# Performance work log

Hardware: AMD Instinct MI355X
Metric: run time of the kernel (lower is better)

The kernel has to match this reference:

```python
import jax, jax.numpy as jnp
from jax import lax
import numpy as np

B, T, NX, NXS, NY, NYS, H = 4096, 60, 4, 3, 4, 3, 128


def lstm(x, h0, c0, Wih, Whh, bih, bhh):
    """PyTorch-convention LSTM. x: [B,T,D] -> (hs [B,T,H], hT, cT). Gate order i,f,g,o."""
    xg = jnp.einsum('btd,gd->btg', x, Wih) + bih  # [B,T,4H] precomputed input gates

    def step(carry, xg_t):
        h, c = carry
        g = xg_t + h @ Whh.T + bhh
        i, f, gg, o = jnp.split(g, 4, axis=-1)
        c = jax.nn.sigmoid(f) * c + jax.nn.sigmoid(i) * jnp.tanh(gg)
        h = jax.nn.sigmoid(o) * jnp.tanh(c)
        return (h, c), h

    (hT, cT), hs = lax.scan(step, (h0, c0), jnp.swapaxes(xg, 0, 1))
    return jnp.swapaxes(hs, 0, 1), hT, cT


def setup_inputs() -> dict:
    key = jax.random.key(0)
    ks = jax.random.split(key, 24)
    s = 0.1  # weight init scale
    inp = {
        'inputs_main': jax.random.normal(ks[0], (B, T, NX), jnp.float32),
        'inputs_sfc': jax.random.normal(ks[1], (B, NXS), jnp.float32),
        'rnn1_mem': jax.random.normal(ks[2], (B, T, H), jnp.float32),
        'hx2': jax.random.normal(ks[3], (B, H), jnp.float32),
        'cx2': jax.random.normal(ks[4], (B, H), jnp.float32),
        # surface MLPs -> initial h/c of rnn1
        'W_sfc1': s * jax.random.normal(ks[5], (H, NXS), jnp.float32),
        'b_sfc1': s * jax.random.normal(ks[6], (H,), jnp.float32),
        'W_sfc2': s * jax.random.normal(ks[7], (H, NXS), jnp.float32),
        'b_sfc2': s * jax.random.normal(ks[8], (H,), jnp.float32),
        # rnn1: input dim nx + nh_mem = 4 + 128 = 132
        'Wih1': s * jax.random.normal(ks[9], (4 * H, NX + H), jnp.float32),
        'Whh1': s * jax.random.normal(ks[10], (4 * H, H), jnp.float32),
        'bih1': s * jax.random.normal(ks[11], (4 * H,), jnp.float32),
        'bhh1': s * jax.random.normal(ks[12], (4 * H,), jnp.float32),
        # rnn2: input dim H
        'Wih2': s * jax.random.normal(ks[13], (4 * H, H), jnp.float32),
        'Whh2': s * jax.random.normal(ks[14], (4 * H, H), jnp.float32),
        'bih2': s * jax.random.normal(ks[15], (4 * H,), jnp.float32),
        'bhh2': s * jax.random.normal(ks[16], (4 * H,), jnp.float32),
        # intermediate + output MLPs
        'W_lat': s * jax.random.normal(ks[17], (H, H), jnp.float32),
        'b_lat': s * jax.random.normal(ks[18], (H,), jnp.float32),
        'W_out': s * jax.random.normal(ks[19], (NY, H), jnp.float32),
        'b_out': s * jax.random.normal(ks[20], (NY,), jnp.float32),
        'W_so': s * jax.random.normal(ks[21], (NYS, H), jnp.float32),
        'b_so': s * jax.random.normal(ks[22], (NYS,), jnp.float32),
    }
    return inp


def reference(inputs_main, inputs_sfc, rnn1_mem, hx2, cx2,
              W_sfc1, b_sfc1, W_sfc2, b_sfc2,
              Wih1, Whh1, bih1, bhh1,
              Wih2, Whh2, bih2, bhh2,
              W_lat, b_lat, W_out, b_out, W_so, b_so):
    # initial states of rnn1 from surface features
    hx = jnp.tanh(inputs_sfc @ W_sfc1.T + b_sfc1)
    cx = jnp.tanh(inputs_sfc @ W_sfc2.T + b_sfc2)
    # flip vertical levels, concat memory feedback
    x = jnp.flip(inputs_main, axis=1)
    x = jnp.concatenate([x, rnn1_mem], axis=2)  # [B,T,NX+H]
    rnn1out, _, _ = lstm(x, hx, cx, Wih1, Whh1, bih1, bhh1)
    rnn1out = jnp.flip(rnn1out, axis=1)
    # second LSTM over the opposite direction, random initial state
    rnn2out, last_h, _ = lstm(rnn1out, hx2, cx2, Wih2, Whh2, bih2, bhh2)
    # intermediate mlp (also becomes next-step memory in the stateful module)
    lat = rnn2out @ W_lat.T + b_lat  # [B,T,H]
    out = lat @ W_out.T + b_out      # [B,T,NY]
    out_sfc = last_h @ W_so.T + b_so  # [B,NYS]
    return out, out_sfc
```

## Files before the change

kernel.cpp:

```cpp
#include <hip/hip_runtime.h>
#include <stdint.h>


typedef __bf16 bf16x8 __attribute__((ext_vector_type(8)));
typedef __bf16 bf16x4 __attribute__((ext_vector_type(4)));
typedef float  f32x4  __attribute__((ext_vector_type(4)));

#define HQ      4096u
#define H0_OFF  0u
#define XD_OFF  8192u
#define XA_OFF  24576u
#define HIST    32256u
#define LDS_SZ  163328
#define NWS     28

#define S1f (-1.4426950408889634f)
#define S2f (-2.8853900817779268f)

__device__ __forceinline__ bf16x8 ldw8s(const float* __restrict__ p, float s){
  float4 a = *(const float4*)p;
  float4 b = *(const float4*)(p+4);
  bf16x8 r;
  r[0]=(__bf16)(a.x*s); r[1]=(__bf16)(a.y*s); r[2]=(__bf16)(a.z*s); r[3]=(__bf16)(a.w*s);
  r[4]=(__bf16)(b.x*s); r[5]=(__bf16)(b.y*s); r[6]=(__bf16)(b.z*s); r[7]=(__bf16)(b.w*s);
  return r;
}
__device__ __forceinline__ void load_wgate(bf16x8 (&dst)[8], const float* pih, const float* phh, int gg, float s){
  #pragma unroll
  for (int kk=0;kk<4;++kk) dst[kk]   = ldw8s(pih + kk*32 + gg*8, s);
  #pragma unroll
  for (int kk=0;kk<4;++kk) dst[4+kk] = ldw8s(phh + kk*32 + gg*8, s);
}
__device__ __forceinline__ void step_barrier(){
  asm volatile("s_waitcnt lgkmcnt(0)\n\ts_barrier" ::: "memory");
}
__device__ __forceinline__ void lstm_pw(const f32x4& a0, const f32x4& a1,
                                        const f32x4& a2, const f32x4& a3,
                                        float (&c_)[4], float (&hn)[4]){
  #pragma unroll
  for (int i=0;i<4;++i){
    float ei = __builtin_amdgcn_exp2f(a0[i]);
    float ef = __builtin_amdgcn_exp2f(a1[i]);
    float eg = __builtin_amdgcn_exp2f(fminf(a2[i], 126.0f));
    float eo = __builtin_amdgcn_exp2f(a3[i]);
    float sf = __builtin_amdgcn_rcpf(1.0f + ef);
    float itg = (1.0f - eg) * __builtin_amdgcn_rcpf((1.0f + ei)*(1.0f + eg));
    float ci = sf*c_[i] + itg;
    float ec = __builtin_amdgcn_exp2f(S2f*__builtin_fabsf(ci));
    float th = (1.0f - ec) * __builtin_amdgcn_rcpf((1.0f + eo)*(1.0f + ec));
    c_[i] = ci;
    hn[i] = __builtin_copysignf(th, ci);
  }
}

__global__ void comb_kernel(const float* __restrict__ W_lat, const float* __restrict__ b_lat,
                            const float* __restrict__ W_out, const float* __restrict__ b_out,
                            float* __restrict__ wcomb){
  int tid = threadIdx.x;
  int m = tid >> 7, k = tid & 127;
  float s = 0.f;
  for (int a=0;a<128;++a) s += W_out[m*128+a]*W_lat[a*128+k];
  wcomb[tid] = s;
  if (tid < 4){
    float sb = b_out[tid];
    for (int a=0;a<128;++a) sb += W_out[tid*128+a]*b_lat[a];
    wcomb[512+tid] = sb;
  }
}

#define MF(af_,wb_,ac_) ac_ = __builtin_amdgcn_mfma_f32_16x16x32_bf16(af_, wb_, ac_, 0,0,0)

#define XPART1(A0_,A1_,A2_,A3_, XB_, TT_) do{ \
    bf16x8 xa_ = {}; \
    if (gg == 0){ bf16x4 x4_ = *(const bf16x4*)(lds + XA_OFF + (uint32_t)((((TT_))<<4)+l16)*8u); \
      xa_[0]=x4_[0]; xa_[1]=x4_[1]; xa_[2]=x4_[2]; xa_[3]=x4_[3]; } \
    A0_ = (f32x4){bias0,bias0,bias0,bias0}; \
    A1_ = (f32x4){bias1,bias1,bias1,bias1}; \
    A2_ = (f32x4){bias2,bias2,bias2,bias2}; \
    A3_ = (f32x4){bias3,bias3,bias3,bias3}; \
    MF(xa_,wxB0,A0_); MF(xa_,wxB1,A1_); MF(xa_,wxB2,A2_); MF(xa_,wxB3,A3_); \
    _Pragma("unroll") \
    for (int kk_=0;kk_<4;++kk_){ \
      uint4 q_ = *(const uint4*)(lds + (XB_) + ((abase + 64u*(uint32_t)kk_) ^ amask)); \
      bf16x8 af_ = __builtin_bit_cast(bf16x8, q_); \
      MF(af_,wB0[kk_],A0_); MF(af_,wB1[kk_],A1_); MF(af_,wB2[kk_],A2_); MF(af_,wB3[kk_],A3_); } \
  }while(0)

#define XPART2(A0_,A1_,A2_,A3_, XB_) do{ \
    A0_ = (f32x4){bias0,bias0,bias0,bias0}; \
    A1_ = (f32x4){bias1,bias1,bias1,bias1}; \
    A2_ = (f32x4){bias2,bias2,bias2,bias2}; \
    A3_ = (f32x4){bias3,bias3,bias3,bias3}; \
    _Pragma("unroll") \
    for (int kk_=0;kk_<4;++kk_){ \
      uint4 q_ = *(const uint4*)(lds + (XB_) + ((abase + 64u*(uint32_t)kk_) ^ amask)); \
      bf16x8 af_ = __builtin_bit_cast(bf16x8, q_); \
      MF(af_,wB0[kk_],A0_); MF(af_,wB1[kk_],A1_); MF(af_,wB2[kk_],A2_); MF(af_,wB3[kk_],A3_); } \
  }while(0)

#define BODY1(T_, CUR_, C0,C1,C2,C3, N0,N1,N2,N3) { \
    const uint32_t Hc_ = H0_OFF + (uint32_t)(CUR_)*HQ; \
    uint4 qh0_ = *(const uint4*)(lds + Hc_ + ((abase       ) ^ amask)); \
    uint4 qh1_ = *(const uint4*)(lds + Hc_ + ((abase +  64u) ^ amask)); \
    uint4 qh2_ = *(const uint4*)(lds + Hc_ + ((abase + 128u) ^ amask)); \
    uint4 qh3_ = *(const uint4*)(lds + Hc_ + ((abase + 192u) ^ amask)); \
    uint2 hv_ = *(const uint2*)(lds + Hc_ + stg_off); \
    if ((T_) < 59){ \
      const int s1_ = (T_) + 1; \
      const uint32_t xb_ = (s1_ >= NWS) ? (HIST + (uint32_t)(s1_-NWS)*HQ) : (XD_OFF + (uint32_t)(s1_&3)*HQ); \
      XPART1(N0,N1,N2,N3, xb_, 58-(T_)); \
    } \
    bf16x8 h0_ = __builtin_bit_cast(bf16x8, qh0_); \
    bf16x8 h1_ = __builtin_bit_cast(bf16x8, qh1_); \
    bf16x8 h2_ = __builtin_bit_cast(bf16x8, qh2_); \
    bf16x8 h3_ = __builtin_bit_cast(bf16x8, qh3_); \
    MF(h0_,wB0[4],C0); MF(h0_,wB1[4],C1); MF(h0_,wB2[4],C2); MF(h0_,wB3[4],C3); \
    MF(h1_,wB0[5],C0); MF(h1_,wB1[5],C1); MF(h1_,wB2[5],C2); MF(h1_,wB3[5],C3); \
    MF(h2_,wB0[6],C0); MF(h2_,wB1[6],C1); MF(h2_,wB2[6],C2); MF(h2_,wB3[6],C3); \
    MF(h3_,wB0[7],C0); MF(h3_,wB1[7],C1); MF(h3_,wB2[7],C2); MF(h3_,wB3[7],C3); \
    float hn_[4]; \
    lstm_pw(C0,C1,C2,C3, c_, hn_); \
    if ((T_) >= 1){ \
      if ((T_) <= NWS) ws_u2[ws_base + (size_t)((T_)-1)*512 + tid] = hv_; \
      else *(uint2*)(lds + HIST + (uint32_t)((T_)-1-NWS)*HQ + stg_off) = hv_; \
    } \
    if ((T_) + 2 <= 59){ \
      const int s2_ = (T_) + 2; \
      const uint32_t sd_ = (s2_ >= NWS) ? (HIST + (uint32_t)(s2_-NWS)*HQ) : (XD_OFF + (uint32_t)(s2_&3)*HQ); \
      bf16x4 m4_; m4_[0]=(__bf16)P0.x; m4_[1]=(__bf16)P0.y; m4_[2]=(__bf16)P0.z; m4_[3]=(__bf16)P0.w; \
      *(bf16x4*)(lds + sd_ + stg_off) = m4_; \
    } \
    _Pragma("unroll") \
    for (int i_=0;i_<4;++i_) \
      *(__bf16*)(lds + H0_OFF + (uint32_t)(1-(CUR_))*HQ + hw_off[i_]) = (__bf16)hn_[i_]; \
    P0 = P1; \
    if ((T_) + 4 <= 59) P1 = *(const float4*)(memrow + (size_t)((T_)+4)*128); \
    step_barrier(); \
  }

#define BODY2(T_, CUR_, C0,C1,C2,C3, N0,N1,N2,N3) { \
    const uint32_t Hc_ = H0_OFF + (uint32_t)(CUR_)*HQ; \
    uint4 qh0_ = *(const uint4*)(lds + Hc_ + ((abase       ) ^ amask)); \
    uint4 qh1_ = *(const uint4*)(lds + Hc_ + ((abase +  64u) ^ amask)); \
    uint4 qh2_ = *(const uint4*)(lds + Hc_ + ((abase + 128u) ^ amask)); \
    uint4 qh3_ = *(const uint4*)(lds + Hc_ + ((abase + 192u) ^ amask)); \
    if ((T_) < 59){ \
      const int s1_ = 58 - (T_); \
      const uint32_t xb_ = (s1_ >= NWS) ? (HIST + (uint32_t)(s1_-NWS)*HQ) : (XD_OFF + (uint32_t)(s1_&3)*HQ); \
      XPART2(N0,N1,N2,N3, xb_); \
    } \
    bf16x8 h0_ = __builtin_bit_cast(bf16x8, qh0_); \
    bf16x8 h1_ = __builtin_bit_cast(bf16x8, qh1_); \
    bf16x8 h2_ = __builtin_bit_cast(bf16x8, qh2_); \
    bf16x8 h3_ = __builtin_bit_cast(bf16x8, qh3_); \
    MF(h0_,wB0[4],C0); MF(h0_,wB1[4],C1); MF(h0_,wB2[4],C2); MF(h0_,wB3[4],C3); \
    MF(h1_,wB0[5],C0); MF(h1_,wB1[5],C1); MF(h1_,wB2[5],C2); MF(h1_,wB3[5],C3); \
    MF(h2_,wB0[6],C0); MF(h2_,wB1[6],C1); MF(h2_,wB2[6],C2); MF(h2_,wB3[6],C3); \
    MF(h3_,wB0[7],C0); MF(h3_,wB1[7],C1); MF(h3_,wB2[7],C2); MF(h3_,wB3[7],C3); \
    f32x4 ao_ = {0.f,0.f,0.f,0.f}; \
    if (w == 0){ MF(h0_,wcB[0],ao_); MF(h1_,wcB[1],ao_); MF(h2_,wcB[2],ao_); MF(h3_,wcB[3],ao_); } \
    float hn_[4]; \
    lstm_pw(C0,C1,C2,C3, c_, hn_); \
    if ((T_) > 0 && w == 0 && l16 < 4){ \
      _Pragma("unroll") \
      for (int i_=0;i_<4;++i_) \
        dout[(size_t)(b0 + gg*4 + i_)*240 + (size_t)((T_)-1)*4 + l16] = ao_[i_] + bc; \
    } \
    if ((T_) >= 29 && (T_) <= 56) \
      *(uint2*)(lds + XD_OFF + (uint32_t)((56-(T_))&3)*HQ + stg_off) = P0u; \
    _Pragma("unroll") \
    for (int i_=0;i_<4;++i_) \
      *(__bf16*)(lds + H0_OFF + (uint32_t)(1-(CUR_))*HQ + hw_off[i_]) = (__bf16)hn_[i_]; \
    P0u = P1u; \
    if ((T_) >= 27 && (T_) <= 54) P1u = ws_u2[ws_base + (size_t)(54-(T_))*512 + tid]; \
    step_barrier(); \
  }

__global__ __launch_bounds__(512, 2)
void lstm_fused(const float* __restrict__ xmain_g, const float* __restrict__ sfc,
                const float* __restrict__ mem_g, const float* __restrict__ hx2g,
                const float* __restrict__ cx2g,
                const float* __restrict__ Wsfc1, const float* __restrict__ bsfc1,
                const float* __restrict__ Wsfc2, const float* __restrict__ bsfc2,
                const float* __restrict__ Wih1, const float* __restrict__ Whh1,
                const float* __restrict__ bih1, const float* __restrict__ bhh1,
                const float* __restrict__ Wih2, const float* __restrict__ Whh2,
                const float* __restrict__ bih2, const float* __restrict__ bhh2,
                const float* __restrict__ Wso, const float* __restrict__ bso,
                const float* __restrict__ wcomb_ws,
                uint2* __restrict__ ws_u2, float* __restrict__ dout)
{
  __shared__ __align__(16) unsigned char lds[LDS_SZ];
  const int tid = threadIdx.x;
  const int w   = tid >> 6;
  const int l   = tid & 63;
  const int gg  = l >> 4;
  const int l16 = l & 15;
  const int blk = blockIdx.x;
  const int b0  = blk * 16;
  const int j   = (w<<4) + l16;
  const uint32_t amask = (uint32_t)((l16 & 7) << 4);
  const uint32_t abase = (uint32_t)(l16*256 + gg*16);
  const int srow = tid >> 5;
  const uint32_t stg_off = (uint32_t)(((srow*256) + (tid&31)*8) ^ ((srow&7)<<4));
  uint32_t hw_off[4];
  #pragma unroll
  for (int i=0;i<4;++i){
    int r = gg*4 + i;
    hw_off[i] = (uint32_t)((r*256 + j*2) ^ ((r&7)<<4));
  }
  const size_t ws_base = (size_t)blk * NWS * 512;

  #pragma unroll
  for (int e = tid; e < 960; e += 512){
    int t = e >> 4, row = e & 15;
    float4 xv = *(const float4*)(xmain_g + (size_t)(b0+row)*240 + t*4);
    bf16x4 b4; b4[0]=(__bf16)xv.x; b4[1]=(__bf16)xv.y; b4[2]=(__bf16)xv.z; b4[3]=(__bf16)xv.w;
    *(bf16x4*)(lds + XA_OFF + (uint32_t)e*8u) = b4;
  }
  const float* memrow = mem_g + (size_t)(b0 + srow)*7680 + (tid&31)*4;
  {
    float4 m0 = *(const float4*)memrow;
    float4 m1 = *(const float4*)(memrow + 128);
    bf16x4 a4; a4[0]=(__bf16)m0.x; a4[1]=(__bf16)m0.y; a4[2]=(__bf16)m0.z; a4[3]=(__bf16)m0.w;
    bf16x4 b4; b4[0]=(__bf16)m1.x; b4[1]=(__bf16)m1.y; b4[2]=(__bf16)m1.z; b4[3]=(__bf16)m1.w;
    *(bf16x4*)(lds + XD_OFF + stg_off) = a4;
    *(bf16x4*)(lds + XD_OFF + HQ + stg_off) = b4;
  }
  {
    int c0 = (tid&31)*4;
    float4 wa = *(const float4*)(Wsfc1 + c0*3);
    float4 wb = *(const float4*)(Wsfc1 + c0*3 + 4);
    float4 wc = *(const float4*)(Wsfc1 + c0*3 + 8);
    const float* sp = sfc + (size_t)(b0+srow)*3;
    float s0 = sp[0], s1 = sp[1], s2 = sp[2];
    float4 bb = *(const float4*)(bsfc1 + c0);
    float v0 = tanhf(bb.x + s0*wa.x + s1*wa.y + s2*wa.z);
    float v1 = tanhf(bb.y + s0*wa.w + s1*wb.x + s2*wb.y);
    float v2 = tanhf(bb.z + s0*wb.z + s1*wb.w + s2*wc.x);
    float v3 = tanhf(bb.w + s0*wc.y + s1*wc.z + s2*wc.w);
    bf16x4 h4; h4[0]=(__bf16)v0; h4[1]=(__bf16)v1; h4[2]=(__bf16)v2; h4[3]=(__bf16)v3;
    *(bf16x4*)(lds + H0_OFF + stg_off) = h4;
  }
  float c_[4];
  {
    const float* wr = Wsfc2 + j*3;
    float w0_=wr[0], w1_=wr[1], w2_=wr[2];
    float bj = bsfc2[j];
    #pragma unroll
    for (int i=0;i<4;++i){
      const float* sp = sfc + (size_t)(b0 + gg*4 + i)*3;
      c_[i] = tanhf(bj + sp[0]*w0_ + sp[1]*w1_ + sp[2]*w2_);
    }
  }
  bf16x8 wB0[8], wB1[8], wB2[8], wB3[8];
  load_wgate(wB0, Wih1 + 4 + (size_t)(0*128+j)*132, Whh1 + (size_t)(0*128+j)*128, gg, S1f);
  load_wgate(wB1, Wih1 + 4 + (size_t)(1*128+j)*132, Whh1 + (size_t)(1*128+j)*128, gg, S1f);
  load_wgate(wB2, Wih1 + 4 + (size_t)(2*128+j)*132, Whh1 + (size_t)(2*128+j)*128, gg, S2f);
  load_wgate(wB3, Wih1 + 4 + (size_t)(3*128+j)*132, Whh1 + (size_t)(3*128+j)*128, gg, S1f);
  bf16x8 wxB0 = {}, wxB1 = {}, wxB2 = {}, wxB3 = {};
  if (gg == 0){
    float4 x0 = *(const float4*)(Wih1 + (size_t)(0*128+j)*132);
    float4 x1 = *(const float4*)(Wih1 + (size_t)(1*128+j)*132);
    float4 x2 = *(const float4*)(Wih1 + (size_t)(2*128+j)*132);
    float4 x3 = *(const float4*)(Wih1 + (size_t)(3*128+j)*132);
    wxB0[0]=(__bf16)(x0.x*S1f); wxB0[1]=(__bf16)(x0.y*S1f); wxB0[2]=(__bf16)(x0.z*S1f); wxB0[3]=(__bf16)(x0.w*S1f);
    wxB1[0]=(__bf16)(x1.x*S1f); wxB1[1]=(__bf16)(x1.y*S1f); wxB1[2]=(__bf16)(x1.z*S1f); wxB1[3]=(__bf16)(x1.w*S1f);
    wxB2[0]=(__bf16)(x2.x*S2f); wxB2[1]=(__bf16)(x2.y*S2f); wxB2[2]=(__bf16)(x2.z*S2f); wxB2[3]=(__bf16)(x2.w*S2f);
    wxB3[0]=(__bf16)(x3.x*S1f); wxB3[1]=(__bf16)(x3.y*S1f); wxB3[2]=(__bf16)(x3.z*S1f); wxB3[3]=(__bf16)(x3.w*S1f);
  }
  float bias0 = (bih1[0*128+j] + bhh1[0*128+j])*S1f;
  float bias1 = (bih1[1*128+j] + bhh1[1*128+j])*S1f;
  float bias2 = (bih1[2*128+j] + bhh1[2*128+j])*S2f;
  float bias3 = (bih1[3*128+j] + bhh1[3*128+j])*S1f;
  float4 P0 = *(const float4*)(memrow + 2*128);
  float4 P1 = *(const float4*)(memrow + 3*128);
  step_barrier();

  f32x4 A0, A1, A2, A3, B0, B1, B2, B3;
  XPART1(A0,A1,A2,A3, XD_OFF, 59);

  #pragma unroll 1
  for (int tb = 0; tb < 60; tb += 2){
    BODY1(tb,   0, A0,A1,A2,A3, B0,B1,B2,B3)
    BODY1(tb+1, 1, B0,B1,B2,B3, A0,A1,A2,A3)
  }
  {
    uint2 hv = *(const uint2*)(lds + H0_OFF + stg_off);
    *(uint2*)(lds + HIST + 31u*HQ + stg_off) = hv;
    float4 h2v = *(const float4*)(hx2g + (size_t)(b0+srow)*128 + (tid&31)*4);
    bf16x4 h4; h4[0]=(__bf16)h2v.x; h4[1]=(__bf16)h2v.y; h4[2]=(__bf16)h2v.z; h4[3]=(__bf16)h2v.w;
    *(bf16x4*)(lds + H0_OFF + stg_off) = h4;
  }
  #pragma unroll
  for (int i=0;i<4;++i) c_[i] = cx2g[(size_t)(b0 + gg*4 + i)*128 + j];
  load_wgate(wB0, Wih2 + (size_t)(0*128+j)*128, Whh2 + (size_t)(0*128+j)*128, gg, S1f);
  load_wgate(wB1, Wih2 + (size_t)(1*128+j)*128, Whh2 + (size_t)(1*128+j)*128, gg, S1f);
  load_wgate(wB2, Wih2 + (size_t)(2*128+j)*128, Whh2 + (size_t)(2*128+j)*128, gg, S2f);
  load_wgate(wB3, Wih2 + (size_t)(3*128+j)*128, Whh2 + (size_t)(3*128+j)*128, gg, S1f);
  float nb0 = (bih2[0*128+j] + bhh2[0*128+j])*S1f;
  float nb1 = (bih2[1*128+j] + bhh2[1*128+j])*S1f;
  float nb2 = (bih2[2*128+j] + bhh2[2*128+j])*S2f;
  float nb3 = (bih2[3*128+j] + bhh2[3*128+j])*S1f;
  bias0=nb0; bias1=nb1; bias2=nb2; bias3=nb3;
  bf16x8 wcB[4] = {};
  if (w == 0){
    #pragma unroll
    for (int kk=0;kk<4;++kk){
      bf16x8 v = {};
      if (l16 < 4) v = ldw8s(wcomb_ws + l16*128 + kk*32 + gg*8, 1.0f);
      wcB[kk] = v;
    }
  }
  const float bc = (l16 < 4) ? wcomb_ws[512 + l16] : 0.f;
  asm volatile("s_waitcnt vmcnt(0) lgkmcnt(0)" ::: "memory");
  __builtin_amdgcn_s_barrier();

  uint2 P0u, P1u;
  XPART2(A0,A1,A2,A3, HIST + 31u*HQ);

  #pragma unroll 1
  for (int tb = 0; tb < 60; tb += 2){
    BODY2(tb,   0, A0,A1,A2,A3, B0,B1,B2,B3)
    BODY2(tb+1, 1, B0,B1,B2,B3, A0,A1,A2,A3)
  }

  if (w == 0){
    bf16x8 wsB[4];
    #pragma unroll
    for (int kk=0;kk<4;++kk){
      bf16x8 v = {};
      if (l16 < 3) v = ldw8s(Wso + l16*128 + kk*32 + gg*8, 1.0f);
      wsB[kk] = v;
    }
    f32x4 ao = {0.f,0.f,0.f,0.f};
    f32x4 as_ = {0.f,0.f,0.f,0.f};
    #pragma unroll
    for (int kk=0;kk<4;++kk){
      uint4 q = *(const uint4*)(lds + H0_OFF + ((abase + 64u*(uint32_t)kk) ^ amask));
      bf16x8 af = __builtin_bit_cast(bf16x8, q);
      ao  = __builtin_amdgcn_mfma_f32_16x16x32_bf16(af, wcB[kk], ao, 0,0,0);
      as_ = __builtin_amdgcn_mfma_f32_16x16x32_bf16(af, wsB[kk], as_, 0,0,0);
    }
    if (l16 < 4){
      #pragma unroll
      for (int i=0;i<4;++i)
        dout[(size_t)(b0 + gg*4 + i)*240 + 59*4 + l16] = ao[i] + bc;
    }
    if (l16 < 3){
      float bs = bso[l16];
      #pragma unroll
      for (int i=0;i<4;++i)
        dout[983040 + (size_t)(b0 + gg*4 + i)*3 + l16] = as_[i] + bs;
    }
  }
}

extern "C" void kernel_launch(void* const* d_in, const int* in_sizes, int n_in,
                              void* d_out, int out_size, void* d_ws, size_t ws_size,
                              hipStream_t stream){
  const float* inputs_main = (const float*)d_in[0];
  const float* inputs_sfc  = (const float*)d_in[1];
  const float* rnn1_mem    = (const float*)d_in[2];
  const float* hx2  = (const float*)d_in[3];
  const float* cx2  = (const float*)d_in[4];
  const float* W_sfc1 = (const float*)d_in[5];
  const float* b_sfc1 = (const float*)d_in[6];
  const float* W_sfc2 = (const float*)d_in[7];
  const float* b_sfc2 = (const float*)d_in[8];
  const float* Wih1 = (const float*)d_in[9];
  const float* Whh1 = (const float*)d_in[10];
  const float* bih1 = (const float*)d_in[11];
  const float* bhh1 = (const float*)d_in[12];
  const float* Wih2 = (const float*)d_in[13];
  const float* Whh2 = (const float*)d_in[14];
  const float* bih2 = (const float*)d_in[15];
  const float* bhh2 = (const float*)d_in[16];
  const float* W_lat = (const float*)d_in[17];
  const float* b_lat = (const float*)d_in[18];
  const float* W_out = (const float*)d_in[19];
  const float* b_out = (const float*)d_in[20];
  const float* W_so  = (const float*)d_in[21];
  const float* b_so  = (const float*)d_in[22];
  float* out = (float*)d_out;
  uint2* ws_u2 = (uint2*)d_ws;
  float* wcomb = (float*)((char*)d_ws + 62914560u);

  comb_kernel<<<dim3(1), dim3(512), 0, stream>>>(W_lat, b_lat, W_out, b_out, wcomb);
  lstm_fused<<<dim3(256), dim3(512), 0, stream>>>(inputs_main, inputs_sfc, rnn1_mem, hx2, cx2,
      W_sfc1, b_sfc1, W_sfc2, b_sfc2, Wih1, Whh1, bih1, bhh1, Wih2, Whh2, bih2, bhh2,
      W_so, b_so, wcomb, ws_u2, out);
}
```

Measured before the change: 198.5 us.

## Spill layer-1 hidden history to global workspace and drop LDS history buffer

Layer 1's hidden-state history now goes entirely to a per-block global workspace, row-major, instead of being split between workspace and a large LDS history region. This shrinks LDS from about 160KB to about 32KB. Layer 2 reads its inputs straight from workspace into registers, two steps ahead. The input-projection MFMAs are no longer precomputed one step early; they run in the same step as the recurrent MFMAs. That puts more MFMA work and LDS reads on each step's critical path, in exchange for smaller LDS and simpler indexing.

```diff
diff --git a/kernel.cpp b/kernel.cpp
--- a/kernel.cpp
+++ b/kernel.cpp
@@ -10,9 +10,7 @@
 #define H0_OFF  0u
 #define XD_OFF  8192u
 #define XA_OFF  24576u
-#define HIST    32256u
-#define LDS_SZ  163328
-#define NWS     28
+#define LDS_SZ  32256
 
 #define S1f (-1.4426950408889634f)
 #define S2f (-2.8853900817779268f)
@@ -69,110 +67,41 @@
 }
 
 #define MF(af_,wb_,ac_) ac_ = __builtin_amdgcn_mfma_f32_16x16x32_bf16(af_, wb_, ac_, 0,0,0)
-
-#define XPART1(A0_,A1_,A2_,A3_, XB_, TT_) do{ \
-    bf16x8 xa_ = {}; \
-    if (gg == 0){ bf16x4 x4_ = *(const bf16x4*)(lds + XA_OFF + (uint32_t)((((TT_))<<4)+l16)*8u); \
-      xa_[0]=x4_[0]; xa_[1]=x4_[1]; xa_[2]=x4_[2]; xa_[3]=x4_[3]; } \
-    A0_ = (f32x4){bias0,bias0,bias0,bias0}; \
-    A1_ = (f32x4){bias1,bias1,bias1,bias1}; \
-    A2_ = (f32x4){bias2,bias2,bias2,bias2}; \
-    A3_ = (f32x4){bias3,bias3,bias3,bias3}; \
-    MF(xa_,wxB0,A0_); MF(xa_,wxB1,A1_); MF(xa_,wxB2,A2_); MF(xa_,wxB3,A3_); \
-    _Pragma("unroll") \
-    for (int kk_=0;kk_<4;++kk_){ \
-      uint4 q_ = *(const uint4*)(lds + (XB_) + ((abase + 64u*(uint32_t)kk_) ^ amask)); \
-      bf16x8 af_ = __builtin_bit_cast(bf16x8, q_); \
-      MF(af_,wB0[kk_],A0_); MF(af_,wB1[kk_],A1_); MF(af_,wB2[kk_],A2_); MF(af_,wB3[kk_],A3_); } \
-  }while(0)
-
-#define XPART2(A0_,A1_,A2_,A3_, XB_) do{ \
-    A0_ = (f32x4){bias0,bias0,bias0,bias0}; \
-    A1_ = (f32x4){bias1,bias1,bias1,bias1}; \
-    A2_ = (f32x4){bias2,bias2,bias2,bias2}; \
-    A3_ = (f32x4){bias3,bias3,bias3,bias3}; \
-    _Pragma("unroll") \
-    for (int kk_=0;kk_<4;++kk_){ \
-      uint4 q_ = *(const uint4*)(lds + (XB_) + ((abase + 64u*(uint32_t)kk_) ^ amask)); \
-      bf16x8 af_ = __builtin_bit_cast(bf16x8, q_); \
-      MF(af_,wB0[kk_],A0_); MF(af_,wB1[kk_],A1_); MF(af_,wB2[kk_],A2_); MF(af_,wB3[kk_],A3_); } \
-  }while(0)
-
-#define BODY1(T_, CUR_, C0,C1,C2,C3, N0,N1,N2,N3) { \
+#define BC8(q_) __builtin_bit_cast(bf16x8, q_)
+
+#define BODY2(T_, CUR_, X0_,X1_,X2_,X3_) { \
     const uint32_t Hc_ = H0_OFF + (uint32_t)(CUR_)*HQ; \
     uint4 qh0_ = *(const uint4*)(lds + Hc_ + ((abase       ) ^ amask)); \
     uint4 qh1_ = *(const uint4*)(lds + Hc_ + ((abase +  64u) ^ amask)); \
     uint4 qh2_ = *(const uint4*)(lds + Hc_ + ((abase + 128u) ^ amask)); \
     uint4 qh3_ = *(const uint4*)(lds + Hc_ + ((abase + 192u) ^ amask)); \
-    uint2 hv_ = *(const uint2*)(lds + Hc_ + stg_off); \
-    if ((T_) < 59){ \
-      const int s1_ = (T_) + 1; \
-      const uint32_t xb_ = (s1_ >= NWS) ? (HIST + (uint32_t)(s1_-NWS)*HQ) : (XD_OFF + (uint32_t)(s1_&3)*HQ); \
-      XPART1(N0,N1,N2,N3, xb_, 58-(T_)); \
+    f32x4 a0 = biasv0, a1 = biasv1, a2 = biasv2, a3 = biasv3; \
+    MF(BC8(X0_),wB0[0],a0); MF(BC8(X0_),wB1[0],a1); MF(BC8(X0_),wB2[0],a2); MF(BC8(X0_),wB3[0],a3); \
+    MF(BC8(X1_),wB0[1],a0); MF(BC8(X1_),wB1[1],a1); MF(BC8(X1_),wB2[1],a2); MF(BC8(X1_),wB3[1],a3); \
+    MF(BC8(X2_),wB0[2],a0); MF(BC8(X2_),wB1[2],a1); MF(BC8(X2_),wB2[2],a2); MF(BC8(X2_),wB3[2],a3); \
+    MF(BC8(X3_),wB0[3],a0); MF(BC8(X3_),wB1[3],a1); MF(BC8(X3_),wB2[3],a2); MF(BC8(X3_),wB3[3],a3); \
+    if ((T_) <= 57){ \
+      const char* xp_ = wsb + (size_t)(57-(T_))*4096u + xfoff; \
+      X0_ = *(const uint4*)(xp_);      X1_ = *(const uint4*)(xp_+64); \
+      X2_ = *(const uint4*)(xp_+128);  X3_ = *(const uint4*)(xp_+192); \
     } \
-    bf16x8 h0_ = __builtin_bit_cast(bf16x8, qh0_); \
-    bf16x8 h1_ = __builtin_bit_cast(bf16x8, qh1_); \
-    bf16x8 h2_ = __builtin_bit_cast(bf16x8, qh2_); \
-    bf16x8 h3_ = __builtin_bit_cast(bf16x8, qh3_); \
-    MF(h0_,wB0[4],C0); MF(h0_,wB1[4],C1); MF(h0_,wB2[4],C2); MF(h0_,wB3[4],C3); \
-    MF(h1_,wB0[5],C0); MF(h1_,wB1[5],C1); MF(h1_,wB2[5],C2); MF(h1_,wB3[5],C3); \
-    MF(h2_,wB0[6],C0); MF(h2_,wB1[6],C1); MF(h2_,wB2[6],C2); MF(h2_,wB3[6],C3); \
-    MF(h3_,wB0[7],C0); MF(h3_,wB1[7],C1); MF(h3_,wB2[7],C2); MF(h3_,wB3[7],C3); \
-    float hn_[4]; \
-    lstm_pw(C0,C1,C2,C3, c_, hn_); \
-    if ((T_) >= 1){ \
-      if ((T_) <= NWS) ws_u2[ws_base + (size_t)((T_)-1)*512 + tid] = hv_; \
-      else *(uint2*)(lds + HIST + (uint32_t)((T_)-1-NWS)*HQ + stg_off) = hv_; \
-    } \
-    if ((T_) + 2 <= 59){ \
-      const int s2_ = (T_) + 2; \
-      const uint32_t sd_ = (s2_ >= NWS) ? (HIST + (uint32_t)(s2_-NWS)*HQ) : (XD_OFF + (uint32_t)(s2_&3)*HQ); \
-      bf16x4 m4_; m4_[0]=(__bf16)P0.x; m4_[1]=(__bf16)P0.y; m4_[2]=(__bf16)P0.z; m4_[3]=(__bf16)P0.w; \
-      *(bf16x4*)(lds + sd_ + stg_off) = m4_; \
-    } \
-    _Pragma("unroll") \
-    for (int i_=0;i_<4;++i_) \
-      *(__bf16*)(lds + H0_OFF + (uint32_t)(1-(CUR_))*HQ + hw_off[i_]) = (__bf16)hn_[i_]; \
-    P0 = P1; \
-    if ((T_) + 4 <= 59) P1 = *(const float4*)(memrow + (size_t)((T_)+4)*128); \
-    step_barrier(); \
-  }
-
-#define BODY2(T_, CUR_, C0,C1,C2,C3, N0,N1,N2,N3) { \
-    const uint32_t Hc_ = H0_OFF + (uint32_t)(CUR_)*HQ; \
-    uint4 qh0_ = *(const uint4*)(lds + Hc_ + ((abase       ) ^ amask)); \
-    uint4 qh1_ = *(const uint4*)(lds + Hc_ + ((abase +  64u) ^ amask)); \
-    uint4 qh2_ = *(const uint4*)(lds + Hc_ + ((abase + 128u) ^ amask)); \
-    uint4 qh3_ = *(const uint4*)(lds + Hc_ + ((abase + 192u) ^ amask)); \
-    if ((T_) < 59){ \
-      const int s1_ = 58 - (T_); \
-      const uint32_t xb_ = (s1_ >= NWS) ? (HIST + (uint32_t)(s1_-NWS)*HQ) : (XD_OFF + (uint32_t)(s1_&3)*HQ); \
-      XPART2(N0,N1,N2,N3, xb_); \
-    } \
-    bf16x8 h0_ = __builtin_bit_cast(bf16x8, qh0_); \
-    bf16x8 h1_ = __builtin_bit_cast(bf16x8, qh1_); \
-    bf16x8 h2_ = __builtin_bit_cast(bf16x8, qh2_); \
-    bf16x8 h3_ = __builtin_bit_cast(bf16x8, qh3_); \
-    MF(h0_,wB0[4],C0); MF(h0_,wB1[4],C1); MF(h0_,wB2[4],C2); MF(h0_,wB3[4],C3); \
-    MF(h1_,wB0[5],C0); MF(h1_,wB1[5],C1); MF(h1_,wB2[5],C2); MF(h1_,wB3[5],C3); \
-    MF(h2_,wB0[6],C0); MF(h2_,wB1[6],C1); MF(h2_,wB2[6],C2); MF(h2_,wB3[6],C3); \
-    MF(h3_,wB0[7],C0); MF(h3_,wB1[7],C1); MF(h3_,wB2[7],C2); MF(h3_,wB3[7],C3); \
+    bf16x8 h0_ = BC8(qh0_), h1_ = BC8(qh1_), h2_ = BC8(qh2_), h3_ = BC8(qh3_); \
+    MF(h0_,wB0[4],a0); MF(h0_,wB1[4],a1); MF(h0_,wB2[4],a2); MF(h0_,wB3[4],a3); \
+    MF(h1_,wB0[5],a0); MF(h1_,wB1[5],a1); MF(h1_,wB2[5],a2); MF(h1_,wB3[5],a3); \
+    MF(h2_,wB0[6],a0); MF(h2_,wB1[6],a1); MF(h2_,wB2[6],a2); MF(h2_,wB3[6],a3); \
+    MF(h3_,wB0[7],a0); MF(h3_,wB1[7],a1); MF(h3_,wB2[7],a2); MF(h3_,wB3[7],a3); \
     f32x4 ao_ = {0.f,0.f,0.f,0.f}; \
     if (w == 0){ MF(h0_,wcB[0],ao_); MF(h1_,wcB[1],ao_); MF(h2_,wcB[2],ao_); MF(h3_,wcB[3],ao_); } \
     float hn_[4]; \
-    lstm_pw(C0,C1,C2,C3, c_, hn_); \
+    lstm_pw(a0,a1,a2,a3, c_, hn_); \
     if ((T_) > 0 && w == 0 && l16 < 4){ \
       _Pragma("unroll") \
       for (int i_=0;i_<4;++i_) \
         dout[(size_t)(b0 + gg*4 + i_)*240 + (size_t)((T_)-1)*4 + l16] = ao_[i_] + bc; \
     } \
-    if ((T_) >= 29 && (T_) <= 56) \
-      *(uint2*)(lds + XD_OFF + (uint32_t)((56-(T_))&3)*HQ + stg_off) = P0u; \
     _Pragma("unroll") \
     for (int i_=0;i_<4;++i_) \
       *(__bf16*)(lds + H0_OFF + (uint32_t)(1-(CUR_))*HQ + hw_off[i_]) = (__bf16)hn_[i_]; \
-    P0u = P1u; \
-    if ((T_) >= 27 && (T_) <= 54) P1u = ws_u2[ws_base + (size_t)(54-(T_))*512 + tid]; \
     step_barrier(); \
   }
 
@@ -209,7 +138,10 @@
     int r = gg*4 + i;
     hw_off[i] = (uint32_t)((r*256 + j*2) ^ ((r&7)<<4));
   }
-  const size_t ws_base = (size_t)blk * NWS * 512;
+  uint2* wsimg = ws_u2 + (size_t)blk * 30720;
+  const uint32_t imgoff = (uint32_t)(srow*32 + (tid&31));
+  const char* wsb = (const char*)(ws_u2 + (size_t)blk * 30720);
+  const uint32_t xfoff = (uint32_t)(l16*256 + gg*16);
 
   #pragma unroll
   for (int e = tid; e < 960; e += 512){
@@ -273,21 +205,61 @@
   float bias1 = (bih1[1*128+j] + bhh1[1*128+j])*S1f;
   float bias2 = (bih1[2*128+j] + bhh1[2*128+j])*S2f;
   float bias3 = (bih1[3*128+j] + bhh1[3*128+j])*S1f;
+  f32x4 biasv0 = {bias0,bias0,bias0,bias0};
+  f32x4 biasv1 = {bias1,bias1,bias1,bias1};
+  f32x4 biasv2 = {bias2,bias2,bias2,bias2};
+  f32x4 biasv3 = {bias3,bias3,bias3,bias3};
   float4 P0 = *(const float4*)(memrow + 2*128);
   float4 P1 = *(const float4*)(memrow + 3*128);
   step_barrier();
 
-  f32x4 A0, A1, A2, A3, B0, B1, B2, B3;
-  XPART1(A0,A1,A2,A3, XD_OFF, 59);
-
   #pragma unroll 1
-  for (int tb = 0; tb < 60; tb += 2){
-    BODY1(tb,   0, A0,A1,A2,A3, B0,B1,B2,B3)
-    BODY1(tb+1, 1, B0,B1,B2,B3, A0,A1,A2,A3)
+  for (int t=0; t<60; ++t){
+    const uint32_t cur = (uint32_t)(t & 1);
+    const uint32_t Hc = H0_OFF + cur*HQ;
+    const uint32_t xb = XD_OFF + (uint32_t)(t & 3)*HQ;
+    uint4 qx0 = *(const uint4*)(lds + xb + ((abase       ) ^ amask));
+    uint4 qx1 = *(const uint4*)(lds + xb + ((abase +  64u) ^ amask));
+    uint4 qx2 = *(const uint4*)(lds + xb + ((abase + 128u) ^ amask));
+    uint4 qx3 = *(const uint4*)(lds + xb + ((abase + 192u) ^ amask));
+    uint4 qh0 = *(const uint4*)(lds + Hc + ((abase       ) ^ amask));
+    uint4 qh1 = *(const uint4*)(lds + Hc + ((abase +  64u) ^ amask));
+    uint4 qh2 = *(const uint4*)(lds + Hc + ((abase + 128u) ^ amask));
+    uint4 qh3 = *(const uint4*)(lds + Hc + ((abase + 192u) ^ amask));
+    uint2 hv  = *(const uint2*)(lds + Hc + stg_off);
+    bf16x8 xa = {};
+    if (gg == 0){
+      bf16x4 x4 = *(const bf16x4*)(lds + XA_OFF + (uint32_t)(((59-t)<<4) + l16)*8u);
+      xa[0]=x4[0]; xa[1]=x4[1]; xa[2]=x4[2]; xa[3]=x4[3];
+    }
+    f32x4 a0 = biasv0, a1 = biasv1, a2 = biasv2, a3 = biasv3;
+    MF(xa,wxB0,a0); MF(xa,wxB1,a1); MF(xa,wxB2,a2); MF(xa,wxB3,a3);
+    MF(BC8(qx0),wB0[0],a0); MF(BC8(qx0),wB1[0],a1); MF(BC8(qx0),wB2[0],a2); MF(BC8(qx0),wB3[0],a3);
+    MF(BC8(qx1),wB0[1],a0); MF(BC8(qx1),wB1[1],a1); MF(BC8(qx1),wB2[1],a2); MF(BC8(qx1),wB3[1],a3);
+    MF(BC8(qx2),wB0[2],a0); MF(BC8(qx2),wB1[2],a1); MF(BC8(qx2),wB2[2],a2); MF(BC8(qx2),wB3[2],a3);
+    MF(BC8(qx3),wB0[3],a0); MF(BC8(qx3),wB1[3],a1); MF(BC8(qx3),wB2[3],a2); MF(BC8(qx3),wB3[3],a3);
+    bf16x8 h0 = BC8(qh0), h1 = BC8(qh1), h2 = BC8(qh2), h3 = BC8(qh3);
+    MF(h0,wB0[4],a0); MF(h0,wB1[4],a1); MF(h0,wB2[4],a2); MF(h0,wB3[4],a3);
+    MF(h1,wB0[5],a0); MF(h1,wB1[5],a1); MF(h1,wB2[5],a2); MF(h1,wB3[5],a3);
+    MF(h2,wB0[6],a0); MF(h2,wB1[6],a1); MF(h2,wB2[6],a2); MF(h2,wB3[6],a3);
+    MF(h3,wB0[7],a0); MF(h3,wB1[7],a1); MF(h3,wB2[7],a2); MF(h3,wB3[7],a3);
+    float hn[4];
+    lstm_pw(a0,a1,a2,a3, c_, hn);
+    if (t >= 1) wsimg[(size_t)(t-1)*512 + imgoff] = hv;
+    if (t + 2 <= 59){
+      bf16x4 m4; m4[0]=(__bf16)P0.x; m4[1]=(__bf16)P0.y; m4[2]=(__bf16)P0.z; m4[3]=(__bf16)P0.w;
+      *(bf16x4*)(lds + XD_OFF + (uint32_t)((t+2)&3)*HQ + stg_off) = m4;
+    }
+    #pragma unroll
+    for (int i=0;i<4;++i)
+      *(__bf16*)(lds + H0_OFF + (1u-cur)*HQ + hw_off[i]) = (__bf16)hn[i];
+    P0 = P1;
+    if (t + 4 <= 59) P1 = *(const float4*)(memrow + (size_t)(t+4)*128);
+    step_barrier();
   }
   {
     uint2 hv = *(const uint2*)(lds + H0_OFF + stg_off);
-    *(uint2*)(lds + HIST + 31u*HQ + stg_off) = hv;
+    wsimg[(size_t)59*512 + imgoff] = hv;
     float4 h2v = *(const float4*)(hx2g + (size_t)(b0+srow)*128 + (tid&31)*4);
     bf16x4 h4; h4[0]=(__bf16)h2v.x; h4[1]=(__bf16)h2v.y; h4[2]=(__bf16)h2v.z; h4[3]=(__bf16)h2v.w;
     *(bf16x4*)(lds + H0_OFF + stg_off) = h4;
@@ -298,11 +270,16 @@
   load_wgate(wB1, Wih2 + (size_t)(1*128+j)*128, Whh2 + (size_t)(1*128+j)*128, gg, S1f);
   load_wgate(wB2, Wih2 + (size_t)(2*128+j)*128, Whh2 + (size_t)(2*128+j)*128, gg, S2f);
   load_wgate(wB3, Wih2 + (size_t)(3*128+j)*128, Whh2 + (size_t)(3*128+j)*128, gg, S1f);
-  float nb0 = (bih2[0*128+j] + bhh2[0*128+j])*S1f;
-  float nb1 = (bih2[1*128+j] + bhh2[1*128+j])*S1f;
-  float nb2 = (bih2[2*128+j] + bhh2[2*128+j])*S2f;
-  float nb3 = (bih2[3*128+j] + bhh2[3*128+j])*S1f;
-  bias0=nb0; bias1=nb1; bias2=nb2; bias3=nb3;
+  {
+    float nb0 = (bih2[0*128+j] + bhh2[0*128+j])*S1f;
+    float nb1 = (bih2[1*128+j] + bhh2[1*128+j])*S1f;
+    float nb2 = (bih2[2*128+j] + bhh2[2*128+j])*S2f;
+    float nb3 = (bih2[3*128+j] + bhh2[3*128+j])*S1f;
+    biasv0 = (f32x4){nb0,nb0,nb0,nb0};
+    biasv1 = (f32x4){nb1,nb1,nb1,nb1};
+    biasv2 = (f32x4){nb2,nb2,nb2,nb2};
+    biasv3 = (f32x4){nb3,nb3,nb3,nb3};
+  }
   bf16x8 wcB[4] = {};
   if (w == 0){
     #pragma unroll
@@ -316,13 +293,20 @@
   asm volatile("s_waitcnt vmcnt(0) lgkmcnt(0)" ::: "memory");
   __builtin_amdgcn_s_barrier();
 
-  uint2 P0u, P1u;
-  XPART2(A0,A1,A2,A3, HIST + 31u*HQ);
+  uint4 xA0, xA1, xA2, xA3, xB0t, xB1t, xB2t, xB3t;
+  {
+    const char* pa = wsb + (size_t)59*4096u + xfoff;
+    const char* pb = wsb + (size_t)58*4096u + xfoff;
+    xA0 = *(const uint4*)(pa);     xA1 = *(const uint4*)(pa+64);
+    xA2 = *(const uint4*)(pa+128); xA3 = *(const uint4*)(pa+192);
+    xB0t = *(const uint4*)(pb);     xB1t = *(const uint4*)(pb+64);
+    xB2t = *(const uint4*)(pb+128); xB3t = *(const uint4*)(pb+192);
+  }
 
   #pragma unroll 1
   for (int tb = 0; tb < 60; tb += 2){
-    BODY2(tb,   0, A0,A1,A2,A3, B0,B1,B2,B3)
-    BODY2(tb+1, 1, B0,B1,B2,B3, A0,A1,A2,A3)
+    BODY2(tb,   0, xA0,xA1,xA2,xA3)
+    BODY2(tb+1, 1, xB0t,xB1t,xB2t,xB3t)
   }
 
   if (w == 0){
@@ -338,9 +322,9 @@
     #pragma unroll
     for (int kk=0;kk<4;++kk){
       uint4 q = *(const uint4*)(lds + H0_OFF + ((abase + 64u*(uint32_t)kk) ^ amask));
-      bf16x8 af = __builtin_bit_cast(bf16x8, q);
-      ao  = __builtin_amdgcn_mfma_f32_16x16x32_bf16(af, wcB[kk], ao, 0,0,0);
-      as_ = __builtin_amdgcn_mfma_f32_16x16x32_bf16(af, wsB[kk], as_, 0,0,0);
+      bf16x8 af = BC8(q);
+      MF(af, wcB[kk], ao);
+      MF(af, wsB[kk], as_);
     }
     if (l16 < 4){
       #pragma unroll
```

After: 228.0 us. 1.15x slower.

## Prefetch next-step input fragments from LDS into registers across the barrier

Applied to the files above, without the earlier changes.

Each LSTM step now issues the LDS reads for the input-projection operands of step t+2 right before the barrier. The barrier waits only on the older LDS ops via a partial lgkmcnt wait, so those reads overlap the barrier and the next step's recurrent MFMAs instead of sitting on the critical path. To keep this safe, the staging of the memory input is pushed one step further ahead, and the prologue stages three slots. This costs extra registers (two sets of uint4 fragments) and relies on exact lgkmcnt counts, which could cause hazards or spills under the 2-block launch bound.

```diff
diff --git a/kernel.cpp b/kernel.cpp
--- a/kernel.cpp
+++ b/kernel.cpp
@@ -31,9 +31,11 @@
   #pragma unroll
   for (int kk=0;kk<4;++kk) dst[4+kk] = ldw8s(phh + kk*32 + gg*8, s);
 }
-__device__ __forceinline__ void step_barrier(){
-  asm volatile("s_waitcnt lgkmcnt(0)\n\ts_barrier" ::: "memory");
-}
+#define BAR0() asm volatile("s_waitcnt lgkmcnt(0)\n\ts_barrier" ::: "memory")
+#define BAR4() asm volatile("s_waitcnt lgkmcnt(4)\n\ts_barrier" ::: "memory")
+#define BAR5() asm volatile("s_waitcnt lgkmcnt(5)\n\ts_barrier" ::: "memory")
+__device__ __forceinline__ void step_barrier(){ BAR0(); }
+
 __device__ __forceinline__ void lstm_pw(const f32x4& a0, const f32x4& a1,
                                         const f32x4& a2, const f32x4& a3,
                                         float (&c_)[4], float (&hn)[4]){
@@ -69,6 +71,14 @@
 }
 
 #define MF(af_,wb_,ac_) ac_ = __builtin_amdgcn_mfma_f32_16x16x32_bf16(af_, wb_, ac_, 0,0,0)
+#define BC8(q_) __builtin_bit_cast(bf16x8, q_)
+#define XSLOT(s_) (((s_) >= NWS) ? (HIST + (uint32_t)((s_)-NWS)*HQ) : (XD_OFF + (uint32_t)((s_)&3)*HQ))
+
+#define PF(X0_,X1_,X2_,X3_, SLOT_) { \
+    X0_ = *(const uint4*)(lds + (SLOT_) + ((abase       ) ^ amask)); \
+    X1_ = *(const uint4*)(lds + (SLOT_) + ((abase +  64u) ^ amask)); \
+    X2_ = *(const uint4*)(lds + (SLOT_) + ((abase + 128u) ^ amask)); \
+    X3_ = *(const uint4*)(lds + (SLOT_) + ((abase + 192u) ^ amask)); }
 
 #define XPART1(A0_,A1_,A2_,A3_, XB_, TT_) do{ \
     bf16x8 xa_ = {}; \
@@ -82,7 +92,7 @@
     _Pragma("unroll") \
     for (int kk_=0;kk_<4;++kk_){ \
       uint4 q_ = *(const uint4*)(lds + (XB_) + ((abase + 64u*(uint32_t)kk_) ^ amask)); \
-      bf16x8 af_ = __builtin_bit_cast(bf16x8, q_); \
+      bf16x8 af_ = BC8(q_); \
       MF(af_,wB0[kk_],A0_); MF(af_,wB1[kk_],A1_); MF(af_,wB2[kk_],A2_); MF(af_,wB3[kk_],A3_); } \
   }while(0)
 
@@ -94,26 +104,44 @@
     _Pragma("unroll") \
     for (int kk_=0;kk_<4;++kk_){ \
       uint4 q_ = *(const uint4*)(lds + (XB_) + ((abase + 64u*(uint32_t)kk_) ^ amask)); \
-      bf16x8 af_ = __builtin_bit_cast(bf16x8, q_); \
+      bf16x8 af_ = BC8(q_); \
       MF(af_,wB0[kk_],A0_); MF(af_,wB1[kk_],A1_); MF(af_,wB2[kk_],A2_); MF(af_,wB3[kk_],A3_); } \
   }while(0)
 
-#define BODY1(T_, CUR_, C0,C1,C2,C3, N0,N1,N2,N3) { \
+#define XPART1R(A0_,A1_,A2_,A3_, X0_,X1_,X2_,X3_, XAV_) do{ \
+    bf16x8 xa_ = {}; \
+    if (gg == 0){ xa_[0]=(XAV_)[0]; xa_[1]=(XAV_)[1]; xa_[2]=(XAV_)[2]; xa_[3]=(XAV_)[3]; } \
+    A0_ = (f32x4){bias0,bias0,bias0,bias0}; \
+    A1_ = (f32x4){bias1,bias1,bias1,bias1}; \
+    A2_ = (f32x4){bias2,bias2,bias2,bias2}; \
+    A3_ = (f32x4){bias3,bias3,bias3,bias3}; \
+    MF(xa_,wxB0,A0_); MF(xa_,wxB1,A1_); MF(xa_,wxB2,A2_); MF(xa_,wxB3,A3_); \
+    MF(BC8(X0_),wB0[0],A0_); MF(BC8(X0_),wB1[0],A1_); MF(BC8(X0_),wB2[0],A2_); MF(BC8(X0_),wB3[0],A3_); \
+    MF(BC8(X1_),wB0[1],A0_); MF(BC8(X1_),wB1[1],A1_); MF(BC8(X1_),wB2[1],A2_); MF(BC8(X1_),wB3[1],A3_); \
+    MF(BC8(X2_),wB0[2],A0_); MF(BC8(X2_),wB1[2],A1_); MF(BC8(X2_),wB2[2],A2_); MF(BC8(X2_),wB3[2],A3_); \
+    MF(BC8(X3_),wB0[3],A0_); MF(BC8(X3_),wB1[3],A1_); MF(BC8(X3_),wB2[3],A2_); MF(BC8(X3_),wB3[3],A3_); \
+  }while(0)
+
+#define XPART2R(A0_,A1_,A2_,A3_, X0_,X1_,X2_,X3_) do{ \
+    A0_ = (f32x4){bias0,bias0,bias0,bias0}; \
+    A1_ = (f32x4){bias1,bias1,bias1,bias1}; \
+    A2_ = (f32x4){bias2,bias2,bias2,bias2}; \
+    A3_ = (f32x4){bias3,bias3,bias3,bias3}; \
+    MF(BC8(X0_),wB0[0],A0_); MF(BC8(X0_),wB1[0],A1_); MF(BC8(X0_),wB2[0],A2_); MF(BC8(X0_),wB3[0],A3_); \
+    MF(BC8(X1_),wB0[1],A0_); MF(BC8(X1_),wB1[1],A1_); MF(BC8(X1_),wB2[1],A2_); MF(BC8(X1_),wB3[1],A3_); \
+    MF(BC8(X2_),wB0[2],A0_); MF(BC8(X2_),wB1[2],A1_); MF(BC8(X2_),wB2[2],A2_); MF(BC8(X2_),wB3[2],A3_); \
+    MF(BC8(X3_),wB0[3],A0_); MF(BC8(X3_),wB1[3],A1_); MF(BC8(X3_),wB2[3],A2_); MF(BC8(X3_),wB3[3],A3_); \
+  }while(0)
+
+#define BODY1(T_, CUR_, C0,C1,C2,C3, N0,N1,N2,N3, Xc0,Xc1,Xc2,Xc3,xac, Xn0,Xn1,Xn2,Xn3,xan) { \
     const uint32_t Hc_ = H0_OFF + (uint32_t)(CUR_)*HQ; \
     uint4 qh0_ = *(const uint4*)(lds + Hc_ + ((abase       ) ^ amask)); \
     uint4 qh1_ = *(const uint4*)(lds + Hc_ + ((abase +  64u) ^ amask)); \
     uint4 qh2_ = *(const uint4*)(lds + Hc_ + ((abase + 128u) ^ amask)); \
     uint4 qh3_ = *(const uint4*)(lds + Hc_ + ((abase + 192u) ^ amask)); \
     uint2 hv_ = *(const uint2*)(lds + Hc_ + stg_off); \
-    if ((T_) < 59){ \
-      const int s1_ = (T_) + 1; \
-      const uint32_t xb_ = (s1_ >= NWS) ? (HIST + (uint32_t)(s1_-NWS)*HQ) : (XD_OFF + (uint32_t)(s1_&3)*HQ); \
-      XPART1(N0,N1,N2,N3, xb_, 58-(T_)); \
-    } \
-    bf16x8 h0_ = __builtin_bit_cast(bf16x8, qh0_); \
-    bf16x8 h1_ = __builtin_bit_cast(bf16x8, qh1_); \
-    bf16x8 h2_ = __builtin_bit_cast(bf16x8, qh2_); \
-    bf16x8 h3_ = __builtin_bit_cast(bf16x8, qh3_); \
+    if ((T_) < 59) XPART1R(N0,N1,N2,N3, Xc0,Xc1,Xc2,Xc3, xac); \
+    bf16x8 h0_ = BC8(qh0_), h1_ = BC8(qh1_), h2_ = BC8(qh2_), h3_ = BC8(qh3_); \
     MF(h0_,wB0[4],C0); MF(h0_,wB1[4],C1); MF(h0_,wB2[4],C2); MF(h0_,wB3[4],C3); \
     MF(h1_,wB0[5],C0); MF(h1_,wB1[5],C1); MF(h1_,wB2[5],C2); MF(h1_,wB3[5],C3); \
     MF(h2_,wB0[6],C0); MF(h2_,wB1[6],C1); MF(h2_,wB2[6],C2); MF(h2_,wB3[6],C3); \
@@ -124,9 +152,9 @@
       if ((T_) <= NWS) ws_u2[ws_base + (size_t)((T_)-1)*512 + tid] = hv_; \
       else *(uint2*)(lds + HIST + (uint32_t)((T_)-1-NWS)*HQ + stg_off) = hv_; \
     } \
-    if ((T_) + 2 <= 59){ \
-      const int s2_ = (T_) + 2; \
-      const uint32_t sd_ = (s2_ >= NWS) ? (HIST + (uint32_t)(s2_-NWS)*HQ) : (XD_OFF + (uint32_t)(s2_&3)*HQ); \
+    if ((T_) + 3 <= 59){ \
+      const int s3_ = (T_) + 3; \
+      const uint32_t sd_ = XSLOT(s3_); \
       bf16x4 m4_; m4_[0]=(__bf16)P0.x; m4_[1]=(__bf16)P0.y; m4_[2]=(__bf16)P0.z; m4_[3]=(__bf16)P0.w; \
       *(bf16x4*)(lds + sd_ + stg_off) = m4_; \
     } \
@@ -134,25 +162,27 @@
     for (int i_=0;i_<4;++i_) \
       *(__bf16*)(lds + H0_OFF + (uint32_t)(1-(CUR_))*HQ + hw_off[i_]) = (__bf16)hn_[i_]; \
     P0 = P1; \
-    if ((T_) + 4 <= 59) P1 = *(const float4*)(memrow + (size_t)((T_)+4)*128); \
-    step_barrier(); \
-  }
-
-#define BODY2(T_, CUR_, C0,C1,C2,C3, N0,N1,N2,N3) { \
+    if ((T_) + 5 <= 59) P1 = *(const float4*)(memrow + (size_t)((T_)+5)*128); \
+    __builtin_amdgcn_sched_barrier(0); \
+    if ((T_) <= 57){ \
+      PF(Xn0,Xn1,Xn2,Xn3, XSLOT((T_)+2)); \
+      xan = *(const bf16x4*)(lds + XA_OFF + (uint32_t)(((57-(T_))<<4)+l16)*8u); \
+      __builtin_amdgcn_sched_barrier(0); \
+      BAR5(); \
+    } else { \
+      __builtin_amdgcn_sched_barrier(0); \
+      BAR0(); \
+    } \
+  }
+
+#define BODY2(T_, CUR_, C0,C1,C2,C3, N0,N1,N2,N3, Xc0,Xc1,Xc2,Xc3, Xn0,Xn1,Xn2,Xn3) { \
     const uint32_t Hc_ = H0_OFF + (uint32_t)(CUR_)*HQ; \
     uint4 qh0_ = *(const uint4*)(lds + Hc_ + ((abase       ) ^ amask)); \
     uint4 qh1_ = *(const uint4*)(lds + Hc_ + ((abase +  64u) ^ amask)); \
     uint4 qh2_ = *(const uint4*)(lds + Hc_ + ((abase + 128u) ^ amask)); \
     uint4 qh3_ = *(const uint4*)(lds + Hc_ + ((abase + 192u) ^ amask)); \
-    if ((T_) < 59){ \
-      const int s1_ = 58 - (T_); \
-      const uint32_t xb_ = (s1_ >= NWS) ? (HIST + (uint32_t)(s1_-NWS)*HQ) : (XD_OFF + (uint32_t)(s1_&3)*HQ); \
-      XPART2(N0,N1,N2,N3, xb_); \
-    } \
-    bf16x8 h0_ = __builtin_bit_cast(bf16x8, qh0_); \
-    bf16x8 h1_ = __builtin_bit_cast(bf16x8, qh1_); \
-    bf16x8 h2_ = __builtin_bit_cast(bf16x8, qh2_); \
-    bf16x8 h3_ = __builtin_bit_cast(bf16x8, qh3_); \
+    if ((T_) < 59) XPART2R(N0,N1,N2,N3, Xc0,Xc1,Xc2,Xc3); \
+    bf16x8 h0_ = BC8(qh0_), h1_ = BC8(qh1_), h2_ = BC8(qh2_), h3_ = BC8(qh3_); \
     MF(h0_,wB0[4],C0); MF(h0_,wB1[4],C1); MF(h0_,wB2[4],C2); MF(h0_,wB3[4],C3); \
     MF(h1_,wB0[5],C0); MF(h1_,wB1[5],C1); MF(h1_,wB2[5],C2); MF(h1_,wB3[5],C3); \
     MF(h2_,wB0[6],C0); MF(h2_,wB1[6],C1); MF(h2_,wB2[6],C2); MF(h2_,wB3[6],C3); \
@@ -173,7 +203,15 @@
       *(__bf16*)(lds + H0_OFF + (uint32_t)(1-(CUR_))*HQ + hw_off[i_]) = (__bf16)hn_[i_]; \
     P0u = P1u; \
     if ((T_) >= 27 && (T_) <= 54) P1u = ws_u2[ws_base + (size_t)(54-(T_))*512 + tid]; \
-    step_barrier(); \
+    __builtin_amdgcn_sched_barrier(0); \
+    if ((T_) <= 57){ \
+      PF(Xn0,Xn1,Xn2,Xn3, XSLOT(57-(T_))); \
+      __builtin_amdgcn_sched_barrier(0); \
+      BAR4(); \
+    } else { \
+      __builtin_amdgcn_sched_barrier(0); \
+      BAR0(); \
+    } \
   }
 
 __global__ __launch_bounds__(512, 2)
@@ -222,10 +260,13 @@
   {
     float4 m0 = *(const float4*)memrow;
     float4 m1 = *(const float4*)(memrow + 128);
+    float4 m2 = *(const float4*)(memrow + 256);
     bf16x4 a4; a4[0]=(__bf16)m0.x; a4[1]=(__bf16)m0.y; a4[2]=(__bf16)m0.z; a4[3]=(__bf16)m0.w;
     bf16x4 b4; b4[0]=(__bf16)m1.x; b4[1]=(__bf16)m1.y; b4[2]=(__bf16)m1.z; b4[3]=(__bf16)m1.w;
+    bf16x4 c4; c4[0]=(__bf16)m2.x; c4[1]=(__bf16)m2.y; c4[2]=(__bf16)m2.z; c4[3]=(__bf16)m2.w;
     *(bf16x4*)(lds + XD_OFF + stg_off) = a4;
     *(bf16x4*)(lds + XD_OFF + HQ + stg_off) = b4;
+    *(bf16x4*)(lds + XD_OFF + 2u*HQ + stg_off) = c4;
   }
   {
     int c0 = (tid&31)*4;
@@ -273,17 +314,21 @@
   float bias1 = (bih1[1*128+j] + bhh1[1*128+j])*S1f;
   float bias2 = (bih1[2*128+j] + bhh1[2*128+j])*S2f;
   float bias3 = (bih1[3*128+j] + bhh1[3*128+j])*S1f;
-  float4 P0 = *(const float4*)(memrow + 2*128);
-  float4 P1 = *(const float4*)(memrow + 3*128);
+  float4 P0 = *(const float4*)(memrow + 3*128);
+  float4 P1 = *(const float4*)(memrow + 4*128);
   step_barrier();
 
   f32x4 A0, A1, A2, A3, B0, B1, B2, B3;
+  uint4 Fa0, Fa1, Fa2, Fa3, Fb0, Fb1, Fb2, Fb3;
+  bf16x4 xaa, xab;
   XPART1(A0,A1,A2,A3, XD_OFF, 59);
+  PF(Fa0,Fa1,Fa2,Fa3, XD_OFF + HQ);
+  xaa = *(const bf16x4*)(lds + XA_OFF + (uint32_t)((58<<4)+l16)*8u);
 
   #pragma unroll 1
   for (int tb = 0; tb < 60; tb += 2){
-    BODY1(tb,   0, A0,A1,A2,A3, B0,B1,B2,B3)
-    BODY1(tb+1, 1, B0,B1,B2,B3, A0,A1,A2,A3)
+    BODY1(tb,   0, A0,A1,A2,A3, B0,B1,B2,B3, Fa0,Fa1,Fa2,Fa3,xaa, Fb0,Fb1,Fb2,Fb3,xab)
+    BODY1(tb+1, 1, B0,B1,B2,B3, A0,A1,A2,A3, Fb0,Fb1,Fb2,Fb3,xab, Fa0,Fa1,Fa2,Fa3,xaa)
   }
   {
     uint2 hv = *(const uint2*)(lds + H0_OFF + stg_off);
@@ -298,11 +343,13 @@
   load_wgate(wB1, Wih2 + (size_t)(1*128+j)*128, Whh2 + (size_t)(1*128+j)*128, gg, S1f);
   load_wgate(wB2, Wih2 + (size_t)(2*128+j)*128, Whh2 + (size_t)(2*128+j)*128, gg, S2f);
   load_wgate(wB3, Wih2 + (size_t)(3*128+j)*128, Whh2 + (size_t)(3*128+j)*128, gg, S1f);
-  float nb0 = (bih2[0*128+j] + bhh2[0*128+j])*S1f;
-  float nb1 = (bih2[1*128+j] + bhh2[1*128+j])*S1f;
-  float nb2 = (bih2[2*128+j] + bhh2[2*128+j])*S2f;
-  float nb3 = (bih2[3*128+j] + bhh2[3*128+j])*S1f;
-  bias0=nb0; bias1=nb1; bias2=nb2; bias3=nb3;
+  {
+    float nb0 = (bih2[0*128+j] + bhh2[0*128+j])*S1f;
+    float nb1 = (bih2[1*128+j] + bhh2[1*128+j])*S1f;
+    float nb2 = (bih2[2*128+j] + bhh2[2*128+j])*S2f;
+    float nb3 = (bih2[3*128+j] + bhh2[3*128+j])*S1f;
+    bias0=nb0; bias1=nb1; bias2=nb2; bias3=nb3;
+  }
   bf16x8 wcB[4] = {};
   if (w == 0){
     #pragma unroll
@@ -318,11 +365,12 @@
 
   uint2 P0u, P1u;
   XPART2(A0,A1,A2,A3, HIST + 31u*HQ);
+  PF(Fa0,Fa1,Fa2,Fa3, HIST + 30u*HQ);
 
   #pragma unroll 1
   for (int tb = 0; tb < 60; tb += 2){
-    BODY2(tb,   0, A0,A1,A2,A3, B0,B1,B2,B3)
-    BODY2(tb+1, 1, B0,B1,B2,B3, A0,A1,A2,A3)
+    BODY2(tb,   0, A0,A1,A2,A3, B0,B1,B2,B3, Fa0,Fa1,Fa2,Fa3, Fb0,Fb1,Fb2,Fb3)
+    BODY2(tb+1, 1, B0,B1,B2,B3, A0,A1,A2,A3, Fb0,Fb1,Fb2,Fb3, Fa0,Fa1,Fa2,Fa3)
   }
 
   if (w == 0){
@@ -338,7 +386,7 @@
     #pragma unroll
     for (int kk=0;kk<4;++kk){
       uint4 q = *(const uint4*)(lds + H0_OFF + ((abase + 64u*(uint32_t)kk) ^ amask));
-      bf16x8 af = __builtin_bit_cast(bf16x8, q);
+      bf16x8 af = BC8(q);
       ao  = __builtin_amdgcn_mfma_f32_16x16x32_bf16(af, wcB[kk], ao, 0,0,0);
       as_ = __builtin_amdgcn_mfma_f32_16x16x32_bf16(af, wsB[kk], as_, 0,0,0);
     }
```

Result: slower. 328.2 us (+65.4%).
